# Optimization experiments

Hardware: AMD Instinct MI355X
Metric: run time of the kernel (lower is better)

The kernel has to match this reference:

```python
import jax, jax.numpy as jnp
import numpy as np

N = 50000
E = 1600000


def gcn_conv(x, W, b, src, dst, edge_weight):
    # PyG GCNConv(normalize=False): h = x @ W.T; msg_e = h[src_e] * w_e;
    # out_i = sum_{e: dst_e = i} msg_e + bias
    h = x @ W.T                                   # [N, C_out]
    msg = h[src]                                  # [E, C_out]
    if edge_weight is not None:
        msg = msg * edge_weight[:, None]
    agg = jax.ops.segment_sum(msg, dst, num_segments=N)  # [N, C_out]
    return agg + b


def batchnorm_eval(x, gamma, beta, mean, var, eps=1e-5):
    inv = gamma * jax.lax.rsqrt(var + eps)
    return (x - mean) * inv + beta


def setup_inputs() -> dict:
    key = jax.random.key(0)
    ks = jax.random.split(key, 16)
    d = {}
    d["x"] = jax.random.normal(ks[0], (N, 128), dtype=jnp.float32)
    d["edge_index"] = jax.random.randint(ks[1], (2, E), 0, N, dtype=jnp.int64)
    d["edge_attr"] = jax.random.uniform(ks[2], (E, 8), dtype=jnp.float32)
    # layer 1: 128 -> 256, layer 2: 256 -> 256, layer 3: 256 -> 256
    s1 = 1.0 / np.sqrt(128.0)
    s2 = 1.0 / np.sqrt(256.0)
    d["W1"] = jax.random.uniform(ks[3], (256, 128), jnp.float32, -s1, s1)
    d["b1"] = jnp.zeros((256,), jnp.float32)
    d["g1"] = jnp.ones((256,), jnp.float32)
    d["beta1"] = jnp.zeros((256,), jnp.float32)
    d["m1"] = jax.random.normal(ks[4], (256,), jnp.float32) * 0.1
    d["v1"] = jax.random.uniform(ks[5], (256,), jnp.float32, minval=0.5, maxval=1.5)
    d["W2"] = jax.random.uniform(ks[6], (256, 256), jnp.float32, -s2, s2)
    d["b2"] = jnp.zeros((256,), jnp.float32)
    d["g2"] = jnp.ones((256,), jnp.float32)
    d["beta2"] = jnp.zeros((256,), jnp.float32)
    d["m2"] = jax.random.normal(ks[7], (256,), jnp.float32) * 0.1
    d["v2"] = jax.random.uniform(ks[8], (256,), jnp.float32, minval=0.5, maxval=1.5)
    d["W3"] = jax.random.uniform(ks[9], (256, 256), jnp.float32, -s2, s2)
    d["b3"] = jnp.zeros((256,), jnp.float32)
    return d


def reference(x, edge_index, edge_attr, W1, b1, g1, beta1, m1, v1,
              W2, b2, g2, beta2, m2, v2, W3, b3):
    src, dst = edge_index[0], edge_index[1]
    ew = jnp.mean(edge_attr, axis=-1)            # [E], torch.mean(edge_attr, dim=-1)
    h = gcn_conv(x, W1, b1, src, dst, ew)
    h = jax.nn.relu(batchnorm_eval(h, g1, beta1, m1, v1))
    h = gcn_conv(h, W2, b2, src, dst, ew)
    h = jax.nn.relu(batchnorm_eval(h, g2, beta2, m2, v2))
    out = gcn_conv(h, W3, b3, src, dst, None)    # last layer: no edge_weight
    return out
```

## Files before the change

kernel.cpp:

```cpp
#include <hip/hip_runtime.h>
#include <cstdint>
#include <cstddef>

#define NN 50000
#define EE 1600000
#define KB ((NN + 127) / 128)
#define PCHUNK 4096
#define SLICE 8064
#define GPAD 32

typedef __attribute__((ext_vector_type(8))) short short8;
typedef __attribute__((ext_vector_type(8))) unsigned short ushort8;
typedef __attribute__((ext_vector_type(4))) float float4v;
typedef __attribute__((ext_vector_type(2))) float floatx2;

__device__ __forceinline__ float bf2f(unsigned short u) {
    union { unsigned int i; float f; } v; v.i = ((unsigned int)u) << 16; return v.f;
}
__device__ __forceinline__ unsigned short f2bf(float f) {
    union { float f; unsigned int i; } v; v.f = f;
    unsigned int r = v.i + 0x7FFF + ((v.i >> 16) & 1);
    return (unsigned short)(r >> 16);
}

__global__ __launch_bounds__(256) void cvt_kernel(const float* __restrict__ in,
                                                  unsigned short* __restrict__ out, int n) {
    int i = (blockIdx.x * 256 + threadIdx.x) * 4;
    if (i + 3 >= n) {
        for (int k = i; k < n; k++) out[k] = f2bf(in[k]);
        return;
    }
    float4 v = *(const float4*)(in + i);
    ushort4 o;
    o.x = f2bf(v.x); o.y = f2bf(v.y); o.z = f2bf(v.z); o.w = f2bf(v.w);
    *(ushort4*)(out + i) = o;
}

__global__ __launch_bounds__(256) void cvt_w_kernel(
    const float* __restrict__ w1, unsigned short* __restrict__ o1,
    const float* __restrict__ w2, unsigned short* __restrict__ o2,
    const float* __restrict__ w3, unsigned short* __restrict__ o3)
{
    int i = (blockIdx.x * 256 + threadIdx.x) * 4;
    const float* in; unsigned short* out;
    if (i < 32768) { in = w1; out = o1; }
    else if (i < 32768 + 65536) { in = w2; out = o2; i -= 32768; }
    else { in = w3; out = o3; i -= 32768 + 65536; }
    float4 v = *(const float4*)(in + i);
    ushort4 o;
    o.x = f2bf(v.x); o.y = f2bf(v.y); o.z = f2bf(v.z); o.w = f2bf(v.w);
    *(ushort4*)(out + i) = o;
}

__global__ __launch_bounds__(256) void passA_kernel(
    const int* __restrict__ src, const int* __restrict__ dst,
    const float* __restrict__ ea, int* __restrict__ gbcnt,
    uint2* __restrict__ tmp, int E)
{
    __shared__ int bh[KB];
    __shared__ int bbase[KB];
    const int t = threadIdx.x;
    const int base_e = blockIdx.x * PCHUNK;
    for (int i = t; i < KB; i += 256) bh[i] = 0;
    __syncthreads();

    unsigned int rlo[16]; int dd[16];
    #pragma unroll
    for (int u = 0; u < 16; u++) {
        int e = base_e + u * 256 + t;
        dd[u] = -1;
        if (e < E) {
            int d = dst[e], s = src[e];
            if ((unsigned)d < NN && (unsigned)s < NN) {
                const float4* p = (const float4*)(ea + (size_t)e * 8);
                float4 a = p[0], b = p[1];
                float w = (a.x + a.y + a.z + a.w + b.x + b.y + b.z + b.w) * 0.125f;
                rlo[u] = (unsigned)s | ((unsigned)f2bf(w) << 16);
                dd[u] = d;
                atomicAdd(&bh[d >> 7], 1);
            }
        }
    }
    __syncthreads();
    for (int i = t; i < KB; i += 256) {
        int c = bh[i];
        bbase[i] = (c > 0) ? atomicAdd(&gbcnt[i * GPAD], c) : 0;
        bh[i] = 0;
    }
    __syncthreads();
    #pragma unroll
    for (int u = 0; u < 16; u++) {
        if (dd[u] >= 0) {
            int b = dd[u] >> 7;
            int pos = bbase[b] + atomicAdd(&bh[b], 1);
            if (pos < SLICE)
                tmp[(size_t)b * SLICE + pos] = (uint2){rlo[u], (unsigned)(dd[u] & 127)};
        }
    }
}

__global__ __launch_bounds__(256) void passB_kernel(
    const uint2* __restrict__ tmp, const int* __restrict__ gbcnt,
    int* __restrict__ rowptr, unsigned int* __restrict__ recs)
{
    __shared__ int cnts[KB];
    __shared__ int lh[128];
    __shared__ int lp[128];
    __shared__ int sboff;
    const int b = blockIdx.x;
    const int t = threadIdx.x;
    for (int i = t; i < KB; i += 256) cnts[i] = gbcnt[i * GPAD];
    if (t < 128) lh[t] = 0;
    __syncthreads();
    if (t == 0) {
        int s = 0;
        for (int i = 0; i < b; i++) s += cnts[i];
        sboff = s;
        if (b == KB - 1) rowptr[NN] = s + cnts[b];
    }
    __syncthreads();
    int cnt = cnts[b]; if (cnt > SLICE) cnt = SLICE;
    const uint2* slice = tmp + (size_t)b * SLICE;
    for (int i = t; i < cnt; i += 256) atomicAdd(&lh[slice[i].y], 1);
    __syncthreads();
    if (t < 128) lp[t] = lh[t];
    __syncthreads();
    #pragma unroll
    for (int off = 1; off < 128; off <<= 1) {
        int v = 0;
        if (t < 128 && t >= off) v = lp[t - off];
        __syncthreads();
        if (t < 128) lp[t] += v;
        __syncthreads();
    }
    const int node0 = b * 128;
    const int nnodes = (NN - node0 < 128) ? (NN - node0) : 128;
    if (t < nnodes) {
        int excl = lp[t] - lh[t] + sboff;
        rowptr[node0 + t] = excl;
        lh[t] = excl;
    }
    __syncthreads();
    for (int i = t; i < cnt; i += 256) {
        uint2 r = slice[i];
        int pos = atomicAdd(&lh[r.y], 1);
        recs[pos] = r.x;
    }
}

template <int C, bool HASW>
__global__ __launch_bounds__(256) void gather_bf(
    const unsigned short* __restrict__ h, const int* __restrict__ rowptr,
    const unsigned int* __restrict__ recs, unsigned short* __restrict__ agg)
{
    int node = blockIdx.x * 4 + (threadIdx.x >> 6);
    int lane = threadIdx.x & 63;
    if (node >= NN) return;
    int beg = rowptr[node], end = rowptr[node + 1];

    float a[8] = {0.f, 0.f, 0.f, 0.f, 0.f, 0.f, 0.f, 0.f};

    const int quar = lane >> 4;
    const int l16  = lane & 15;
    int j = beg;
    for (; j + 16 <= end; j += 16) {
        unsigned int r[4]; ushort8 v[4];
        #pragma unroll
        for (int u = 0; u < 4; u++) r[u] = recs[j + 4 * u + quar];
        #pragma unroll
        for (int u = 0; u < 4; u++)
            v[u] = *(const ushort8*)(h + (size_t)(r[u] & 0xFFFF) * 128 + l16 * 8);
        #pragma unroll
        for (int u = 0; u < 4; u++) {
            float w = HASW ? bf2f((unsigned short)(r[u] >> 16)) : 1.f;
            #pragma unroll
            for (int k = 0; k < 8; k++) a[k] += w * bf2f(v[u][k]);
        }
    }
    for (; j < end; j += 4) {
        int idx = j + quar;
        unsigned int r = recs[idx < end ? idx : end - 1];
        float w = (idx < end) ? (HASW ? bf2f((unsigned short)(r >> 16)) : 1.f) : 0.f;
        ushort8 v = *(const ushort8*)(h + (size_t)(r & 0xFFFF) * 128 + l16 * 8);
        #pragma unroll
        for (int k = 0; k < 8; k++) a[k] += w * bf2f(v[k]);
    }
    #pragma unroll
    for (int k = 0; k < 8; k++) {
        a[k] += __shfl_xor(a[k], 16, 64);
        a[k] += __shfl_xor(a[k], 32, 64);
    }
    if (quar == 0) {
        ushort8 o;
        #pragma unroll
        for (int k = 0; k < 8; k++) o[k] = f2bf(a[k]);
        *(ushort8*)(agg + (size_t)node * 128 + l16 * 8) = o;
    }
}

template <bool HASW>
__global__ __launch_bounds__(256) void gather_fp8(
    const unsigned char* __restrict__ h, const int* __restrict__ rowptr,
    const unsigned int* __restrict__ recs, unsigned short* __restrict__ agg)
{
    int node = blockIdx.x * 4 + (threadIdx.x >> 6);
    int lane = threadIdx.x & 63;
    if (node >= NN) return;
    int beg = rowptr[node], end = rowptr[node + 1];

    const int slot = lane >> 4;
    const int l16  = lane & 15;

    float a[16];
    #pragma unroll
    for (int k = 0; k < 16; k++) a[k] = 0.f;

    int j = beg;
    for (; j + 16 <= end; j += 16) {
        unsigned int r[4]; uint4 v[4];
        #pragma unroll
        for (int u = 0; u < 4; u++) r[u] = recs[j + 4 * u + slot];
        #pragma unroll
        for (int u = 0; u < 4; u++)
            v[u] = *(const uint4*)(h + (size_t)(r[u] & 0xFFFF) * 256 + l16 * 16);
        #pragma unroll
        for (int u = 0; u < 4; u++) {
            float w = HASW ? bf2f((unsigned short)(r[u] >> 16)) : 1.f;
            unsigned int ww[4] = {v[u].x, v[u].y, v[u].z, v[u].w};
            #pragma unroll
            for (int wi = 0; wi < 4; wi++) {
                floatx2 lo = __builtin_amdgcn_cvt_pk_f32_fp8(ww[wi], false);
                floatx2 hi = __builtin_amdgcn_cvt_pk_f32_fp8(ww[wi], true);
                a[4 * wi + 0] += w * lo.x;
                a[4 * wi + 1] += w * lo.y;
                a[4 * wi + 2] += w * hi.x;
                a[4 * wi + 3] += w * hi.y;
            }
        }
    }
    for (; j < end; j += 4) {
        int idx = j + slot;
        unsigned int r = recs[idx < end ? idx : end - 1];
        float w = (idx < end) ? (HASW ? bf2f((unsigned short)(r >> 16)) : 1.f) : 0.f;
        uint4 v = *(const uint4*)(h + (size_t)(r & 0xFFFF) * 256 + l16 * 16);
        unsigned int ww[4] = {v.x, v.y, v.z, v.w};
        #pragma unroll
        for (int wi = 0; wi < 4; wi++) {
            floatx2 lo = __builtin_amdgcn_cvt_pk_f32_fp8(ww[wi], false);
            floatx2 hi = __builtin_amdgcn_cvt_pk_f32_fp8(ww[wi], true);
            a[4 * wi + 0] += w * lo.x;
            a[4 * wi + 1] += w * lo.y;
            a[4 * wi + 2] += w * hi.x;
            a[4 * wi + 3] += w * hi.y;
        }
    }
    #pragma unroll
    for (int k = 0; k < 16; k++) {
        a[k] += __shfl_xor(a[k], 16, 64);
        a[k] += __shfl_xor(a[k], 32, 64);
    }
    if (slot == 0) {
        ushort8 o0, o1;
        #pragma unroll
        for (int k = 0; k < 8; k++) { o0[k] = f2bf(a[k]); o1[k] = f2bf(a[k + 8]); }
        *(ushort8*)(agg + (size_t)node * 256 + l16 * 16) = o0;
        *(ushort8*)(agg + (size_t)node * 256 + l16 * 16 + 8) = o1;
    }
}

template <int CIN, int MODE>
__global__ __launch_bounds__(256) void mm_mfma(
    const unsigned short* __restrict__ A, const unsigned short* __restrict__ W,
    const float* __restrict__ bias,
    const float* __restrict__ gamma, const float* __restrict__ beta,
    const float* __restrict__ mean, const float* __restrict__ var,
    void* __restrict__ out, int M)
{
    const int lane = threadIdx.x & 63;
    const int wave = threadIdx.x >> 6;
    const int quad = lane >> 4;
    const int l16  = lane & 15;
    const int row0 = blockIdx.x * 128 + (wave & 1) * 64;
    const int col0 = blockIdx.y * 128 + (wave >> 1) * 64;

    float4v acc[4][4] = {};

    for (int k0 = 0; k0 < CIN; k0 += 32) {
        const int ka = k0 + quad * 8;
        short8 af[4], bf[4];
        #pragma unroll
        for (int i = 0; i < 4; i++) {
            int r = row0 + i * 16 + l16;
            af[i] = (r < M) ? *(const short8*)(A + (size_t)r * CIN + ka) : (short8)0;
            bf[i] = *(const short8*)(W + (size_t)(col0 + i * 16 + l16) * CIN + ka);
        }
        #pragma unroll
        for (int mi = 0; mi < 4; mi++)
            #pragma unroll
            for (int ni = 0; ni < 4; ni++)
                acc[mi][ni] = __builtin_amdgcn_mfma_f32_16x16x32_bf16(
                    af[mi], bf[ni], acc[mi][ni], 0, 0, 0);
    }

    float cb[4], cmu[4], cinv[4], cbe[4];
    #pragma unroll
    for (int ni = 0; ni < 4; ni++) {
        int gc = col0 + ni * 16 + l16;
        cb[ni] = bias[gc];
        if (MODE == 1) {
            cmu[ni]  = mean[gc];
            cinv[ni] = gamma[gc] * rsqrtf(var[gc] + 1e-5f);
            cbe[ni]  = beta[gc];
        }
    }
    #pragma unroll
    for (int mi = 0; mi < 4; mi++) {
        #pragma unroll
        for (int reg = 0; reg < 4; reg++) {
            int gr = row0 + mi * 16 + quad * 4 + reg;
            if (gr >= M) continue;
            #pragma unroll
            for (int ni = 0; ni < 4; ni++) {
                int gc = col0 + ni * 16 + l16;
                float v = acc[mi][ni][reg] + cb[ni];
                if (MODE == 1) {
                    v = (v - cmu[ni]) * cinv[ni] + cbe[ni];
                    v = fmaxf(v, 0.f);
                    int pk = __builtin_amdgcn_cvt_pk_fp8_f32(v, v, 0, false);
                    ((unsigned char*)out)[(size_t)gr * 256 + gc] = (unsigned char)(pk & 0xFF);
                } else {
                    ((float*)out)[(size_t)gr * 256 + gc] = v;
                }
            }
        }
    }
}

extern "C" void kernel_launch(void* const* d_in, const int* in_sizes, int n_in,
                              void* d_out, int out_size, void* d_ws, size_t ws_size,
                              hipStream_t stream) {
    const float* x   = (const float*)d_in[0];
    const int*   ei  = (const int*)d_in[1];
    const float* ea  = (const float*)d_in[2];
    const float* W1  = (const float*)d_in[3];
    const float* b1  = (const float*)d_in[4];
    const float* g1  = (const float*)d_in[5];
    const float* be1 = (const float*)d_in[6];
    const float* m1  = (const float*)d_in[7];
    const float* v1  = (const float*)d_in[8];
    const float* W2  = (const float*)d_in[9];
    const float* b2  = (const float*)d_in[10];
    const float* g2  = (const float*)d_in[11];
    const float* be2 = (const float*)d_in[12];
    const float* m2  = (const float*)d_in[13];
    const float* v2  = (const float*)d_in[14];
    const float* W3  = (const float*)d_in[15];
    const float* b3  = (const float*)d_in[16];

    const int* src = ei;
    const int* dst = ei + EE;

    char* p = (char*)d_ws;
    auto alloc = [&](size_t bytes) { char* r = p; p += (bytes + 255) & ~255ULL; return r; };
    int*            rowptr    = (int*)alloc((NN + 1) * 4);
    int*            gbcnt     = (int*)alloc((size_t)KB * GPAD * 4);
    unsigned int*   recs      = (unsigned int*)alloc((size_t)EE * 4);
    unsigned short* xb        = (unsigned short*)alloc((size_t)NN * 128 * 2);
    unsigned short* W1b       = (unsigned short*)alloc(256 * 128 * 2);
    unsigned short* W2b       = (unsigned short*)alloc(256 * 256 * 2);
    unsigned short* W3b       = (unsigned short*)alloc(256 * 256 * 2);
    unsigned short* agg       = (unsigned short*)alloc((size_t)NN * 256 * 2);
    unsigned char*  hbuf      = (unsigned char*)alloc((size_t)NN * 256);
    float*          out       = (float*)d_out;

    uint2* tmp = (uint2*)agg;

    const int gblocks = (NN + 3) / 4;
    const int mtiles  = (NN + 127) / 128;
    const int pblocks = (EE + PCHUNK - 1) / PCHUNK;

    cvt_kernel<<<(NN * 128 / 4 + 255) / 256, 256, 0, stream>>>(x, xb, NN * 128);
    cvt_w_kernel<<<(32768 + 65536 + 65536) / 4 / 256, 256, 0, stream>>>(
        W1, W1b, W2, W2b, W3, W3b);

    hipMemsetAsync(gbcnt, 0, (size_t)KB * GPAD * 4, stream);
    passA_kernel<<<pblocks, 256, 0, stream>>>(src, dst, ea, gbcnt, tmp, EE);
    passB_kernel<<<KB, 256, 0, stream>>>(tmp, gbcnt, rowptr, recs);

    gather_bf<128, true><<<gblocks, 256, 0, stream>>>(xb, rowptr, recs, agg);
    mm_mfma<128, 1><<<dim3(mtiles, 2), 256, 0, stream>>>(
        agg, W1b, b1, g1, be1, m1, v1, hbuf, NN);

    gather_fp8<true><<<gblocks, 256, 0, stream>>>(hbuf, rowptr, recs, agg);
    mm_mfma<256, 1><<<dim3(mtiles, 2), 256, 0, stream>>>(
        agg, W2b, b2, g2, be2, m2, v2, hbuf, NN);

    gather_fp8<false><<<gblocks, 256, 0, stream>>>(hbuf, rowptr, recs, agg);
    mm_mfma<256, 0><<<dim3(mtiles, 2), 256, 0, stream>>>(
        agg, W3b, b3, nullptr, nullptr, nullptr, nullptr, out, NN);
}
```

Measured before the change: 459.7 us.

## Merge conversion kernels and memset, persistent gather grid, reshape GEMM tiling

After: 456.3 us. No clear change (-0.7%).

```diff
diff --git a/kernel.cpp b/kernel.cpp
--- a/kernel.cpp
+++ b/kernel.cpp
@@ -8,6 +8,7 @@
 #define PCHUNK 4096
 #define SLICE 8064
 #define GPAD 32
+#define GBLK 2048
 
 typedef __attribute__((ext_vector_type(8))) short short8;
 typedef __attribute__((ext_vector_type(8))) unsigned short ushort8;
@@ -23,33 +24,34 @@
     return (unsigned short)(r >> 16);
 }
 
-__global__ __launch_bounds__(256) void cvt_kernel(const float* __restrict__ in,
-                                                  unsigned short* __restrict__ out, int n) {
-    int i = (blockIdx.x * 256 + threadIdx.x) * 4;
-    if (i + 3 >= n) {
-        for (int k = i; k < n; k++) out[k] = f2bf(in[k]);
-        return;
-    }
-    float4 v = *(const float4*)(in + i);
-    ushort4 o;
-    o.x = f2bf(v.x); o.y = f2bf(v.y); o.z = f2bf(v.z); o.w = f2bf(v.w);
-    *(ushort4*)(out + i) = o;
-}
-
-__global__ __launch_bounds__(256) void cvt_w_kernel(
+__global__ __launch_bounds__(256) void cvt_all_kernel(
+    const float* __restrict__ x, unsigned short* __restrict__ xb,
     const float* __restrict__ w1, unsigned short* __restrict__ o1,
     const float* __restrict__ w2, unsigned short* __restrict__ o2,
-    const float* __restrict__ w3, unsigned short* __restrict__ o3)
-{
-    int i = (blockIdx.x * 256 + threadIdx.x) * 4;
-    const float* in; unsigned short* out;
-    if (i < 32768) { in = w1; out = o1; }
-    else if (i < 32768 + 65536) { in = w2; out = o2; i -= 32768; }
-    else { in = w3; out = o3; i -= 32768 + 65536; }
-    float4 v = *(const float4*)(in + i);
-    ushort4 o;
-    o.x = f2bf(v.x); o.y = f2bf(v.y); o.z = f2bf(v.z); o.w = f2bf(v.w);
-    *(ushort4*)(out + i) = o;
+    const float* __restrict__ w3, unsigned short* __restrict__ o3,
+    int* __restrict__ gbcnt)
+{
+    const int blk = blockIdx.x;
+    if (blk < 6250) {
+        int i = (blk * 256 + threadIdx.x) * 4;
+        float4 v = *(const float4*)(x + i);
+        ushort4 o;
+        o.x = f2bf(v.x); o.y = f2bf(v.y); o.z = f2bf(v.z); o.w = f2bf(v.w);
+        *(ushort4*)(xb + i) = o;
+    } else if (blk < 6410) {
+        int i = ((blk - 6250) * 256 + threadIdx.x) * 4;
+        const float* in; unsigned short* out;
+        if (i < 32768) { in = w1; out = o1; }
+        else if (i < 32768 + 65536) { in = w2; out = o2; i -= 32768; }
+        else { in = w3; out = o3; i -= 32768 + 65536; }
+        float4 v = *(const float4*)(in + i);
+        ushort4 o;
+        o.x = f2bf(v.x); o.y = f2bf(v.y); o.z = f2bf(v.z); o.w = f2bf(v.w);
+        *(ushort4*)(out + i) = o;
+    } else {
+        int i = (blk - 6410) * 256 + threadIdx.x;
+        if (i < KB * GPAD) gbcnt[i] = 0;
+    }
 }
 
 __global__ __launch_bounds__(256) void passA_kernel(
@@ -148,53 +150,53 @@
     }
 }
 
-template <int C, bool HASW>
+template <bool HASW>
 __global__ __launch_bounds__(256) void gather_bf(
     const unsigned short* __restrict__ h, const int* __restrict__ rowptr,
     const unsigned int* __restrict__ recs, unsigned short* __restrict__ agg)
 {
-    int node = blockIdx.x * 4 + (threadIdx.x >> 6);
-    int lane = threadIdx.x & 63;
-    if (node >= NN) return;
-    int beg = rowptr[node], end = rowptr[node + 1];
-
-    float a[8] = {0.f, 0.f, 0.f, 0.f, 0.f, 0.f, 0.f, 0.f};
-
+    const int wave = threadIdx.x >> 6;
+    const int lane = threadIdx.x & 63;
     const int quar = lane >> 4;
     const int l16  = lane & 15;
-    int j = beg;
-    for (; j + 16 <= end; j += 16) {
-        unsigned int r[4]; ushort8 v[4];
-        #pragma unroll
-        for (int u = 0; u < 4; u++) r[u] = recs[j + 4 * u + quar];
-        #pragma unroll
-        for (int u = 0; u < 4; u++)
-            v[u] = *(const ushort8*)(h + (size_t)(r[u] & 0xFFFF) * 128 + l16 * 8);
-        #pragma unroll
-        for (int u = 0; u < 4; u++) {
-            float w = HASW ? bf2f((unsigned short)(r[u] >> 16)) : 1.f;
-            #pragma unroll
-            for (int k = 0; k < 8; k++) a[k] += w * bf2f(v[u][k]);
-        }
-    }
-    for (; j < end; j += 4) {
-        int idx = j + quar;
-        unsigned int r = recs[idx < end ? idx : end - 1];
-        float w = (idx < end) ? (HASW ? bf2f((unsigned short)(r >> 16)) : 1.f) : 0.f;
-        ushort8 v = *(const ushort8*)(h + (size_t)(r & 0xFFFF) * 128 + l16 * 8);
-        #pragma unroll
-        for (int k = 0; k < 8; k++) a[k] += w * bf2f(v[k]);
-    }
-    #pragma unroll
-    for (int k = 0; k < 8; k++) {
-        a[k] += __shfl_xor(a[k], 16, 64);
-        a[k] += __shfl_xor(a[k], 32, 64);
-    }
-    if (quar == 0) {
-        ushort8 o;
-        #pragma unroll
-        for (int k = 0; k < 8; k++) o[k] = f2bf(a[k]);
-        *(ushort8*)(agg + (size_t)node * 128 + l16 * 8) = o;
+
+    for (int node = blockIdx.x * 4 + wave; node < NN; node += GBLK * 4) {
+        int beg = rowptr[node], end = rowptr[node + 1];
+        float a[8] = {0.f, 0.f, 0.f, 0.f, 0.f, 0.f, 0.f, 0.f};
+        int j = beg;
+        for (; j + 16 <= end; j += 16) {
+            unsigned int r[4]; ushort8 v[4];
+            #pragma unroll
+            for (int u = 0; u < 4; u++) r[u] = recs[j + 4 * u + quar];
+            #pragma unroll
+            for (int u = 0; u < 4; u++)
+                v[u] = *(const ushort8*)(h + (size_t)(r[u] & 0xFFFF) * 128 + l16 * 8);
+            #pragma unroll
+            for (int u = 0; u < 4; u++) {
+                float w = HASW ? bf2f((unsigned short)(r[u] >> 16)) : 1.f;
+                #pragma unroll
+                for (int k = 0; k < 8; k++) a[k] += w * bf2f(v[u][k]);
+            }
+        }
+        for (; j < end; j += 4) {
+            int idx = j + quar;
+            unsigned int r = recs[idx < end ? idx : end - 1];
+            float w = (idx < end) ? (HASW ? bf2f((unsigned short)(r >> 16)) : 1.f) : 0.f;
+            ushort8 v = *(const ushort8*)(h + (size_t)(r & 0xFFFF) * 128 + l16 * 8);
+            #pragma unroll
+            for (int k = 0; k < 8; k++) a[k] += w * bf2f(v[k]);
+        }
+        #pragma unroll
+        for (int k = 0; k < 8; k++) {
+            a[k] += __shfl_xor(a[k], 16, 64);
+            a[k] += __shfl_xor(a[k], 32, 64);
+        }
+        if (quar == 0) {
+            ushort8 o;
+            #pragma unroll
+            for (int k = 0; k < 8; k++) o[k] = f2bf(a[k]);
+            *(ushort8*)(agg + (size_t)node * 128 + l16 * 8) = o;
+        }
     }
 }
 
@@ -203,30 +205,45 @@
     const unsigned char* __restrict__ h, const int* __restrict__ rowptr,
     const unsigned int* __restrict__ recs, unsigned short* __restrict__ agg)
 {
-    int node = blockIdx.x * 4 + (threadIdx.x >> 6);
-    int lane = threadIdx.x & 63;
-    if (node >= NN) return;
-    int beg = rowptr[node], end = rowptr[node + 1];
-
+    const int wave = threadIdx.x >> 6;
+    const int lane = threadIdx.x & 63;
     const int slot = lane >> 4;
     const int l16  = lane & 15;
 
-    float a[16];
-    #pragma unroll
-    for (int k = 0; k < 16; k++) a[k] = 0.f;
-
-    int j = beg;
-    for (; j + 16 <= end; j += 16) {
-        unsigned int r[4]; uint4 v[4];
-        #pragma unroll
-        for (int u = 0; u < 4; u++) r[u] = recs[j + 4 * u + slot];
-        #pragma unroll
-        for (int u = 0; u < 4; u++)
-            v[u] = *(const uint4*)(h + (size_t)(r[u] & 0xFFFF) * 256 + l16 * 16);
-        #pragma unroll
-        for (int u = 0; u < 4; u++) {
-            float w = HASW ? bf2f((unsigned short)(r[u] >> 16)) : 1.f;
-            unsigned int ww[4] = {v[u].x, v[u].y, v[u].z, v[u].w};
+    for (int node = blockIdx.x * 4 + wave; node < NN; node += GBLK * 4) {
+        int beg = rowptr[node], end = rowptr[node + 1];
+        float a[16];
+        #pragma unroll
+        for (int k = 0; k < 16; k++) a[k] = 0.f;
+        int j = beg;
+        for (; j + 16 <= end; j += 16) {
+            unsigned int r[4]; uint4 v[4];
+            #pragma unroll
+            for (int u = 0; u < 4; u++) r[u] = recs[j + 4 * u + slot];
+            #pragma unroll
+            for (int u = 0; u < 4; u++)
+                v[u] = *(const uint4*)(h + (size_t)(r[u] & 0xFFFF) * 256 + l16 * 16);
+            #pragma unroll
+            for (int u = 0; u < 4; u++) {
+                float w = HASW ? bf2f((unsigned short)(r[u] >> 16)) : 1.f;
+                unsigned int ww[4] = {v[u].x, v[u].y, v[u].z, v[u].w};
+                #pragma unroll
+                for (int wi = 0; wi < 4; wi++) {
+                    floatx2 lo = __builtin_amdgcn_cvt_pk_f32_fp8(ww[wi], false);
+                    floatx2 hi = __builtin_amdgcn_cvt_pk_f32_fp8(ww[wi], true);
+                    a[4 * wi + 0] += w * lo.x;
+                    a[4 * wi + 1] += w * lo.y;
+                    a[4 * wi + 2] += w * hi.x;
+                    a[4 * wi + 3] += w * hi.y;
+                }
+            }
+        }
+        for (; j < end; j += 4) {
+            int idx = j + slot;
+            unsigned int r = recs[idx < end ? idx : end - 1];
+            float w = (idx < end) ? (HASW ? bf2f((unsigned short)(r >> 16)) : 1.f) : 0.f;
+            uint4 v = *(const uint4*)(h + (size_t)(r & 0xFFFF) * 256 + l16 * 16);
+            unsigned int ww[4] = {v.x, v.y, v.z, v.w};
             #pragma unroll
             for (int wi = 0; wi < 4; wi++) {
                 floatx2 lo = __builtin_amdgcn_cvt_pk_f32_fp8(ww[wi], false);
@@ -237,34 +254,18 @@
                 a[4 * wi + 3] += w * hi.y;
             }
         }
-    }
-    for (; j < end; j += 4) {
-        int idx = j + slot;
-        unsigned int r = recs[idx < end ? idx : end - 1];
-        float w = (idx < end) ? (HASW ? bf2f((unsigned short)(r >> 16)) : 1.f) : 0.f;
-        uint4 v = *(const uint4*)(h + (size_t)(r & 0xFFFF) * 256 + l16 * 16);
-        unsigned int ww[4] = {v.x, v.y, v.z, v.w};
-        #pragma unroll
-        for (int wi = 0; wi < 4; wi++) {
-            floatx2 lo = __builtin_amdgcn_cvt_pk_f32_fp8(ww[wi], false);
-            floatx2 hi = __builtin_amdgcn_cvt_pk_f32_fp8(ww[wi], true);
-            a[4 * wi + 0] += w * lo.x;
-            a[4 * wi + 1] += w * lo.y;
-            a[4 * wi + 2] += w * hi.x;
-            a[4 * wi + 3] += w * hi.y;
-        }
-    }
-    #pragma unroll
-    for (int k = 0; k < 16; k++) {
-        a[k] += __shfl_xor(a[k], 16, 64);
-        a[k] += __shfl_xor(a[k], 32, 64);
-    }
-    if (slot == 0) {
-        ushort8 o0, o1;
-        #pragma unroll
-        for (int k = 0; k < 8; k++) { o0[k] = f2bf(a[k]); o1[k] = f2bf(a[k + 8]); }
-        *(ushort8*)(agg + (size_t)node * 256 + l16 * 16) = o0;
-        *(ushort8*)(agg + (size_t)node * 256 + l16 * 16 + 8) = o1;
+        #pragma unroll
+        for (int k = 0; k < 16; k++) {
+            a[k] += __shfl_xor(a[k], 16, 64);
+            a[k] += __shfl_xor(a[k], 32, 64);
+        }
+        if (slot == 0) {
+            ushort8 o0, o1;
+            #pragma unroll
+            for (int k = 0; k < 8; k++) { o0[k] = f2bf(a[k]); o1[k] = f2bf(a[k + 8]); }
+            *(ushort8*)(agg + (size_t)node * 256 + l16 * 16) = o0;
+            *(ushort8*)(agg + (size_t)node * 256 + l16 * 16 + 8) = o1;
+        }
     }
 }
 
@@ -280,8 +281,8 @@
     const int wave = threadIdx.x >> 6;
     const int quad = lane >> 4;
     const int l16  = lane & 15;
-    const int row0 = blockIdx.x * 128 + (wave & 1) * 64;
-    const int col0 = blockIdx.y * 128 + (wave >> 1) * 64;
+    const int row0 = blockIdx.x * 64;
+    const int col0 = wave * 64;
 
     float4v acc[4][4] = {};
 
@@ -375,27 +376,23 @@
 
     uint2* tmp = (uint2*)agg;
 
-    const int gblocks = (NN + 3) / 4;
-    const int mtiles  = (NN + 127) / 128;
+    const int mtiles  = (NN + 63) / 64;
     const int pblocks = (EE + PCHUNK - 1) / PCHUNK;
 
-    cvt_kernel<<<(NN * 128 / 4 + 255) / 256, 256, 0, stream>>>(x, xb, NN * 128);
-    cvt_w_kernel<<<(32768 + 65536 + 65536) / 4 / 256, 256, 0, stream>>>(
-        W1, W1b, W2, W2b, W3, W3b);
-
-    hipMemsetAsync(gbcnt, 0, (size_t)KB * GPAD * 4, stream);
+    cvt_all_kernel<<<6459, 256, 0, stream>>>(x, xb, W1, W1b, W2, W2b, W3, W3b, gbcnt);
+
     passA_kernel<<<pblocks, 256, 0, stream>>>(src, dst, ea, gbcnt, tmp, EE);
     passB_kernel<<<KB, 256, 0, stream>>>(tmp, gbcnt, rowptr, recs);
 
-    gather_bf<128, true><<<gblocks, 256, 0, stream>>>(xb, rowptr, recs, agg);
-    mm_mfma<128, 1><<<dim3(mtiles, 2), 256, 0, stream>>>(
+    gather_bf<true><<<GBLK, 256, 0, stream>>>(xb, rowptr, recs, agg);
+    mm_mfma<128, 1><<<mtiles, 256, 0, stream>>>(
         agg, W1b, b1, g1, be1, m1, v1, hbuf, NN);
 
-    gather_fp8<true><<<gblocks, 256, 0, stream>>>(hbuf, rowptr, recs, agg);
-    mm_mfma<256, 1><<<dim3(mtiles, 2), 256, 0, stream>>>(
+    gather_fp8<true><<<GBLK, 256, 0, stream>>>(hbuf, rowptr, recs, agg);
+    mm_mfma<256, 1><<<mtiles, 256, 0, stream>>>(
         agg, W2b, b2, g2, be2, m2, v2, hbuf, NN);
 
-    gather_fp8<false><<<gblocks, 256, 0, stream>>>(hbuf, rowptr, recs, agg);
-    mm_mfma<256, 0><<<dim3(mtiles, 2), 256, 0, stream>>>(
+    gather_fp8<false><<<GBLK, 256, 0, stream>>>(hbuf, rowptr, recs, agg);
+    mm_mfma<256, 0><<<mtiles, 256, 0, stream>>>(
         agg, W3b, b3, nullptr, nullptr, nullptr, nullptr, out, NN);
 }
```
